# Kernel tuning notes

Measured on AMD Instinct MI355X. Metric: run time of the kernel, lower is better.

Reference implementation:

```python
import jax, jax.numpy as jnp
import numpy as np

B, S, D = 4, 2048, 2048
E = 8            # num_experts
TOP_K = 2
H = 1408         # intermediate_size per expert
SH = 2 * H       # shared expert intermediate (shared_experts=2)


def setup_inputs() -> dict:
    key = jax.random.key(0)
    ks = jax.random.split(key, 8)
    sc = 0.02
    return {
        "hidden_states": jax.random.normal(ks[0], (B, S, D), jnp.float32),
        "gate_w": jax.random.normal(ks[1], (E, D), jnp.float32) * sc,   # torch Linear weight [out,in]
        "w1": jax.random.normal(ks[2], (E, H, D), jnp.float32) * sc,    # gate_proj per expert
        "w3": jax.random.normal(ks[3], (E, H, D), jnp.float32) * sc,    # up_proj per expert
        "w2": jax.random.normal(ks[4], (E, D, H), jnp.float32) * sc,    # down_proj per expert
        "sw1": jax.random.normal(ks[5], (SH, D), jnp.float32) * sc,
        "sw3": jax.random.normal(ks[6], (SH, D), jnp.float32) * sc,
        "sw2": jax.random.normal(ks[7], (D, SH), jnp.float32) * sc,
    }


def reference(hidden_states, gate_w, w1, w3, w2, sw1, sw3, sw2):
    b, s, d = hidden_states.shape
    x = hidden_states.reshape(-1, d)                      # [T, D]
    logits = x @ gate_w.T                                 # [T, E]
    rw, sel = jax.lax.top_k(logits, TOP_K)                # [T, K]
    rw = jax.nn.softmax(rw, axis=-1)                      # norm_topk_prob=True
    onehot = jax.nn.one_hot(sel, E, dtype=x.dtype)        # [T, K, E]
    token_mask = onehot.sum(axis=1)                       # [T, E] in {0,1}
    # NOTE: faithful to the source quirk: expert_weights.sum(dim=-1) on a flat
    # masked gather sums routing weights over ALL tokens selecting the expert,
    # producing one scalar per expert.
    s_e = (rw[..., None] * onehot).sum(axis=(0, 1))       # [E]
    combine = token_mask * s_e                            # [T, E]
    # per-expert SwiGLU MLP on all tokens (dense combine form of gather/scatter)
    g = jnp.einsum('td,ehd->eth', x, w1)                  # [E, T, H]
    u = jnp.einsum('td,ehd->eth', x, w3)
    a = jax.nn.silu(g) * u
    y = jnp.einsum('eth,edh->etd', a, w2)                 # [E, T, D]
    out = jnp.einsum('te,etd->td', combine, y)            # [T, D]
    shared = (jax.nn.silu(x @ sw1.T) * (x @ sw3.T)) @ sw2.T
    out = out + shared
    return out.reshape(b, s, d)
```

## Files before the change

### kernel.cpp

```cpp
#include <hip/hip_runtime.h>
#include <hip/hip_bf16.h>
#include <stdint.h>

#define T_TOK 8192
#define DIM   2048
#define NEXP  8
#define HDIM  1408
#define SHDIM 2816

typedef __attribute__((ext_vector_type(8))) short bfrag;
typedef __attribute__((ext_vector_type(4))) float f32x4;
typedef __attribute__((ext_vector_type(4))) short s16x4;

__device__ __forceinline__ short f2bf(float f) {
    union { float f; uint32_t u; } v; v.f = f;
    return (short)((v.u + 0x8000u) >> 16);
}
__device__ __forceinline__ float bf2f(short s) {
    union { uint32_t u; float f; } v; v.u = ((uint32_t)(uint16_t)s) << 16;
    return v.f;
}

__device__ __forceinline__ bfrag cvt8(float4 a, float4 b) {
    bfrag r;
    r[0] = f2bf(a.x); r[1] = f2bf(a.y); r[2] = f2bf(a.z); r[3] = f2bf(a.w);
    r[4] = f2bf(b.x); r[5] = f2bf(b.y); r[6] = f2bf(b.z); r[7] = f2bf(b.w);
    return r;
}

__device__ __forceinline__ void gload16(const void* g, void* l) {
    __builtin_amdgcn_global_load_lds(
        (__attribute__((address_space(1))) void*)(g),
        (__attribute__((address_space(3))) void*)(l), 16, 0, 0);
}

#define MFMA16(a, b, c) __builtin_amdgcn_mfma_f32_16x16x32_bf16((a), (b), (c), 0, 0, 0)


__global__ __launch_bounds__(256) void gate_cvt_kernel(
    const float* __restrict__ x, const float* __restrict__ gw,
    __hip_bfloat16* __restrict__ xbf,
    int* __restrict__ sel, int* __restrict__ meta, float* __restrict__ s_e,
    const float* __restrict__ sw1f, const float* __restrict__ sw3f,
    const float* __restrict__ sw2f,
    __hip_bfloat16* __restrict__ sw1bf, __hip_bfloat16* __restrict__ sw3bf,
    __hip_bfloat16* __restrict__ sw2bf)
{
    const int bid = blockIdx.x;
    if (bid >= T_TOK / 32) {
        constexpr size_t E_SW = (size_t)SHDIM * DIM;
        constexpr int NCH = (int)(3 * E_SW / 2048);
        const int w = bid - T_TOK / 32;
        for (int c = w; c < NCH; c += 256) {
            size_t elem = (size_t)c * 2048 + threadIdx.x * 8;
            const float* s; __hip_bfloat16* d;
            if      (elem < E_SW)     { s = sw1f + elem;             d = sw1bf + elem; }
            else if (elem < 2 * E_SW) { s = sw3f + (elem - E_SW);    d = sw3bf + (elem - E_SW); }
            else                      { s = sw2f + (elem - 2 * E_SW); d = sw2bf + (elem - 2 * E_SW); }
            float4 a = ((const float4*)s)[0], b = ((const float4*)s)[1];
            *(bfrag*)d = cvt8(a, b);
        }
        return;
    }
    __shared__ float g[NEXP * DIM];
    for (int i = threadIdx.x; i < NEXP * DIM; i += 256) g[i] = gw[i];
    __syncthreads();
    const int wid = threadIdx.x >> 6, lane = threadIdx.x & 63;
    for (int it = 0; it < 8; ++it) {
        const int t = bid * 32 + wid * 8 + it;
        float acc[NEXP];
#pragma unroll
        for (int e = 0; e < NEXP; ++e) acc[e] = 0.f;
        const float4* xr = (const float4*)(x + (size_t)t * DIM);
        for (int j = 0; j < DIM / 4; j += 64) {
            float4 xv = xr[j + lane];
            s16x4 xv16 = { f2bf(xv.x), f2bf(xv.y), f2bf(xv.z), f2bf(xv.w) };
            *(s16x4*)&xbf[(size_t)t * DIM + (j + lane) * 4] = xv16;
#pragma unroll
            for (int e = 0; e < NEXP; ++e) {
                float4 gv = *(const float4*)&g[e * DIM + (j + lane) * 4];
                acc[e] += xv.x * gv.x + xv.y * gv.y + xv.z * gv.z + xv.w * gv.w;
            }
        }
#pragma unroll
        for (int e = 0; e < NEXP; ++e)
            for (int o = 32; o; o >>= 1) acc[e] += __shfl_xor(acc[e], o);
        if (lane == 0) {
            int e0 = 0; float v0 = acc[0];
#pragma unroll
            for (int e = 1; e < NEXP; ++e) if (acc[e] > v0) { v0 = acc[e]; e0 = e; }
            int e1 = -1; float v1 = -3.4e38f;
#pragma unroll
            for (int e = 0; e < NEXP; ++e) if (e != e0 && acc[e] > v1) { v1 = acc[e]; e1 = e; }
            float p0 = 1.f / (1.f + __expf(v1 - v0));
            float p1 = 1.f - p0;
            sel[2 * t] = e0; sel[2 * t + 1] = e1;
            atomicAdd(&s_e[e0], p0); atomicAdd(&s_e[e1], p1);
            atomicAdd(&meta[e0], 1); atomicAdd(&meta[e1], 1);
        }
    }
}

__global__ void scan_kernel(int* meta) {
    if (threadIdx.x == 0) {
        int acc = 0;
        for (int e = 0; e < NEXP; ++e) {
            meta[16 + e] = acc;
            meta[8 + e]  = acc;
            acc += meta[e];
        }
        meta[24] = acc;
    }
}

__global__ __launch_bounds__(256) void fill_kernel(
    const int* __restrict__ sel, int* __restrict__ meta,
    int* __restrict__ list, int2* __restrict__ slots)
{
    const int t = blockIdx.x * 256 + threadIdx.x;
    int e0 = sel[2 * t], e1 = sel[2 * t + 1];
    int p0 = atomicAdd(&meta[8 + e0], 1); list[p0] = t;
    int p1 = atomicAdd(&meta[8 + e1], 1); list[p1] = t;
    slots[t] = make_int2(p0, p1);
}


template<int N, bool GATHER>
__device__ __forceinline__ void up_core(
    const __hip_bfloat16* __restrict__ X,
    const __hip_bfloat16* __restrict__ B1p,
    const __hip_bfloat16* __restrict__ B3p,
    __hip_bfloat16* __restrict__ actp,
    const int* __restrict__ list,
    int base, int count, int m0, int n0, short* lds)
{
    constexpr int K = DIM;
    constexpr int NT = K / 64;
    short (*As)[256 * 64]  = (short (*)[256 * 64])lds;
    short (*B1s)[128 * 64] = (short (*)[128 * 64])(lds + 32768);
    short (*B3s)[128 * 64] = (short (*)[128 * 64])(lds + 49152);

    const int tid = threadIdx.x, wid = tid >> 6, lane = tid & 63;
    const int rlo = lane >> 3;
    const int swslot = (lane & 7) ^ rlo;

    const __hip_bfloat16* pA[4];
#pragma unroll
    for (int q = 0; q < 4; ++q) {
        int row = (q * 8 + wid) * 8 + rlo;
        int r = m0 + row; if (r > count - 1) r = count - 1;
        int ga = GATHER ? list[base + r] : r;
        pA[q] = X + (size_t)ga * K + swslot * 8;
    }
    const __hip_bfloat16* pB1[2];
    const __hip_bfloat16* pB3[2];
#pragma unroll
    for (int q = 0; q < 2; ++q) {
        int row = (q * 8 + wid) * 8 + rlo;
        pB1[q] = B1p + (size_t)(n0 + row) * K + swslot * 8;
        pB3[q] = B3p + (size_t)(n0 + row) * K + swslot * 8;
    }

#define STAGE_UP(T, BUF) do { const int k0_ = (T) * 64;                         \
    _Pragma("unroll") for (int q = 0; q < 4; ++q)                               \
        gload16(pA[q] + k0_, &As[BUF][(q * 8 + wid) * 512]);                    \
    _Pragma("unroll") for (int q = 0; q < 2; ++q) {                             \
        gload16(pB1[q] + k0_, &B1s[BUF][(q * 8 + wid) * 512]);                  \
        gload16(pB3[q] + k0_, &B3s[BUF][(q * 8 + wid) * 512]); } } while (0)

    const int wm = wid >> 2, wn = wid & 3;
    const int l15 = lane & 15, lhi = lane >> 4;

    f32x4 accg[8][2], accu[8][2];
#pragma unroll
    for (int i = 0; i < 8; ++i)
#pragma unroll
        for (int j = 0; j < 2; ++j) { accg[i][j] = 0.f; accu[i][j] = 0.f; }

    STAGE_UP(0, 0);
    __syncthreads();
    int cur = 0;
#pragma unroll 1
    for (int t = 0; t < NT; ++t) {
        if (t + 1 < NT) STAGE_UP(t + 1, cur ^ 1);
        __builtin_amdgcn_sched_barrier(0);
        bfrag b1f[2][2], b3f[2][2];
#pragma unroll
        for (int j = 0; j < 2; ++j)
#pragma unroll
            for (int kk = 0; kk < 2; ++kk) {
                int rb = wn * 32 + j * 16 + l15;
                int c = kk * 4 + lhi;
                int off = rb * 128 + ((c ^ (rb & 7)) << 4);
                b1f[j][kk] = *(const bfrag*)((const char*)B1s[cur] + off);
                b3f[j][kk] = *(const bfrag*)((const char*)B3s[cur] + off);
            }
        __builtin_amdgcn_s_setprio(1);
#pragma unroll
        for (int i = 0; i < 8; ++i) {
            int ra = wm * 128 + i * 16 + l15;
            const char* abase = (const char*)As[cur] + ra * 128;
            bfrag a0 = *(const bfrag*)(abase + ((lhi       ^ (ra & 7)) << 4));
            bfrag a1 = *(const bfrag*)(abase + (((4 + lhi) ^ (ra & 7)) << 4));
#pragma unroll
            for (int j = 0; j < 2; ++j) {
                accg[i][j] = MFMA16(a0, b1f[j][0], accg[i][j]);
                accu[i][j] = MFMA16(a0, b3f[j][0], accu[i][j]);
                accg[i][j] = MFMA16(a1, b1f[j][1], accg[i][j]);
                accu[i][j] = MFMA16(a1, b3f[j][1], accu[i][j]);
            }
        }
        __builtin_amdgcn_s_setprio(0);
        __syncthreads();
        cur ^= 1;
    }
#undef STAGE_UP

#pragma unroll
    for (int i = 0; i < 8; ++i)
#pragma unroll
        for (int r = 0; r < 4; ++r) {
            int m = wm * 128 + i * 16 + lhi * 4 + r;
            if (m0 + m < count) {
#pragma unroll
                for (int j = 0; j < 2; ++j) {
                    float gg = accg[i][j][r];
                    float uu = accu[i][j][r];
                    float a = gg / (1.f + __expf(-gg)) * uu;
                    int n = n0 + wn * 32 + j * 16 + l15;
                    actp[(size_t)(base + m0 + m) * N + n] = __float2bfloat16(a);
                }
            }
        }
}

template<int KD, bool TO_BF16>
__device__ __forceinline__ void down_core(
    const __hip_bfloat16* __restrict__ Ap,
    const __hip_bfloat16* __restrict__ Bp,
    float* __restrict__ out, __hip_bfloat16* __restrict__ yscr,
    int base, int count, int m0, int n0, short* lds)
{
    constexpr int NT = KD / 64;
    short (*As)[256 * 64] = (short (*)[256 * 64])lds;
    short (*Bs)[256 * 64] = (short (*)[256 * 64])(lds + 32768);

    const int tid = threadIdx.x, wid = tid >> 6, lane = tid & 63;
    const int rlo = lane >> 3;
    const int swslot = (lane & 7) ^ rlo;

    const __hip_bfloat16* pA[4];
    const __hip_bfloat16* pB[4];
#pragma unroll
    for (int q = 0; q < 4; ++q) {
        int row = (q * 8 + wid) * 8 + rlo;
        int r = m0 + row; if (r > count - 1) r = count - 1;
        pA[q] = Ap + (size_t)(base + r) * KD + swslot * 8;
        pB[q] = Bp + (size_t)(n0 + row) * KD + swslot * 8;
    }

#define STAGE_DN(T, BUF) do { const int k0_ = (T) * 64;                         \
    _Pragma("unroll") for (int q = 0; q < 4; ++q) {                             \
        gload16(pA[q] + k0_, &As[BUF][(q * 8 + wid) * 512]);                    \
        gload16(pB[q] + k0_, &Bs[BUF][(q * 8 + wid) * 512]); } } while (0)

    const int wm = wid >> 2, wn = wid & 3;
    const int l15 = lane & 15, lhi = lane >> 4;

    f32x4 acc[8][4];
#pragma unroll
    for (int i = 0; i < 8; ++i)
#pragma unroll
        for (int j = 0; j < 4; ++j) acc[i][j] = 0.f;

    STAGE_DN(0, 0);
    __syncthreads();
    int cur = 0;
#pragma unroll 1
    for (int t = 0; t < NT; ++t) {
        if (t + 1 < NT) STAGE_DN(t + 1, cur ^ 1);
        __builtin_amdgcn_sched_barrier(0);
        bfrag bf[4][2];
#pragma unroll
        for (int j = 0; j < 4; ++j)
#pragma unroll
            for (int kk = 0; kk < 2; ++kk) {
                int rb = wn * 64 + j * 16 + l15;
                int c = kk * 4 + lhi;
                bf[j][kk] = *(const bfrag*)((const char*)Bs[cur] + rb * 128 + ((c ^ (rb & 7)) << 4));
            }
        __builtin_amdgcn_s_setprio(1);
#pragma unroll
        for (int i = 0; i < 8; ++i) {
            int ra = wm * 128 + i * 16 + l15;
            const char* abase = (const char*)As[cur] + ra * 128;
            bfrag a0 = *(const bfrag*)(abase + ((lhi       ^ (ra & 7)) << 4));
            bfrag a1 = *(const bfrag*)(abase + (((4 + lhi) ^ (ra & 7)) << 4));
#pragma unroll
            for (int j = 0; j < 4; ++j) {
                acc[i][j] = MFMA16(a0, bf[j][0], acc[i][j]);
                acc[i][j] = MFMA16(a1, bf[j][1], acc[i][j]);
            }
        }
        __builtin_amdgcn_s_setprio(0);
        __syncthreads();
        cur ^= 1;
    }
#undef STAGE_DN

#pragma unroll
    for (int i = 0; i < 8; ++i)
#pragma unroll
        for (int r = 0; r < 4; ++r) {
            int m = wm * 128 + i * 16 + lhi * 4 + r;
            if (m0 + m < count) {
#pragma unroll
                for (int j = 0; j < 4; ++j) {
                    int n = n0 + wn * 64 + j * 16 + l15;
                    if (TO_BF16)
                        yscr[(size_t)(base + m0 + m) * DIM + n] = __float2bfloat16(acc[i][j][r]);
                    else
                        out[(size_t)(m0 + m) * DIM + n] = acc[i][j][r];
                }
            }
        }
}

#define UPSH_NG 704
#define UPSH_NCVT 384
__global__ __launch_bounds__(512, 2) void upsh_cvt_k(
    const __hip_bfloat16* __restrict__ X,
    const __hip_bfloat16* __restrict__ SW1, const __hip_bfloat16* __restrict__ SW3,
    __hip_bfloat16* __restrict__ act_sh,
    const float* __restrict__ w1f, const float* __restrict__ w3f,
    __hip_bfloat16* __restrict__ w1bf, __hip_bfloat16* __restrict__ w3bf)
{
    const int bid = blockIdx.x;
    if (bid >= UPSH_NG) {
        constexpr size_t E_W = (size_t)NEXP * HDIM * DIM;
        constexpr int NCH = (int)(2 * E_W / 4096);
        const int w = bid - UPSH_NG;
        for (int c = w; c < NCH; c += UPSH_NCVT) {
            size_t elem = (size_t)c * 4096 + threadIdx.x * 8;
            const float* s; __hip_bfloat16* d;
            if (elem < E_W) { s = w1f + elem;         d = w1bf + elem; }
            else            { s = w3f + (elem - E_W); d = w3bf + (elem - E_W); }
            float4 a = ((const float4*)s)[0], b = ((const float4*)s)[1];
            *(bfrag*)d = cvt8(a, b);
        }
        return;
    }
    constexpr int nx = SHDIM / 128, cpx = UPSH_NG / 8;
    const int virt = (bid & 7) * cpx + (bid >> 3);
    const int xi = virt % nx, yi = virt / nx;
    __shared__ alignas(16) short lds[65536];
    up_core<SHDIM, false>(X, SW1, SW3, act_sh, nullptr, 0, T_TOK, yi * 256, xi * 128, lds);
}

template<int KD, bool TO_BF16>
__global__ __launch_bounds__(512, 2) void down_k(
    const __hip_bfloat16* __restrict__ A, const __hip_bfloat16* __restrict__ W2,
    float* __restrict__ out, __hip_bfloat16* __restrict__ yscr,
    const int* __restrict__ meta)
{
    constexpr int nx = DIM / 256, ny = T_TOK / 256, nz = TO_BF16 ? NEXP : 1;
    constexpr int nwg = nx * ny * nz, cpx = nwg / 8;
    const int bid = (int)blockIdx.x + nx * ((int)blockIdx.y + ny * (int)blockIdx.z);
    const int virt = (bid & 7) * cpx + (bid >> 3);
    const int xi = virt % nx, rest = virt / nx, yi = rest % ny, e = rest / ny;
    int count, base;
    if (TO_BF16) { count = meta[e]; base = meta[16 + e]; if (yi * 256 >= count) return; }
    else { count = T_TOK; base = 0; }
    __shared__ alignas(16) short lds[65536];
    down_core<KD, TO_BF16>(A, W2 + (size_t)e * DIM * KD, out, yscr,
                           base, count, yi * 256, xi * 256, lds);
}

template<int N, bool GATHER>
__global__ __launch_bounds__(512, 2) void up_k(
    const __hip_bfloat16* __restrict__ X,
    const __hip_bfloat16* __restrict__ W1, const __hip_bfloat16* __restrict__ W3,
    __hip_bfloat16* __restrict__ act,
    const int* __restrict__ list, const int* __restrict__ meta)
{
    constexpr int nx = N / 128, ny = T_TOK / 256, nz = GATHER ? NEXP : 1;
    constexpr int nwg = nx * ny * nz, cpx = nwg / 8;
    const int bid = (int)blockIdx.x + nx * ((int)blockIdx.y + ny * (int)blockIdx.z);
    const int virt = (bid & 7) * cpx + (bid >> 3);
    const int xi = virt % nx, rest = virt / nx, yi = rest % ny, e = rest / ny;
    int count, base;
    if (GATHER) { count = meta[e]; base = meta[16 + e]; if (yi * 256 >= count) return; }
    else { count = T_TOK; base = 0; }
    __shared__ alignas(16) short lds[65536];
    up_core<N, GATHER>(X, W1 + (size_t)e * N * DIM, W3 + (size_t)e * N * DIM,
                       act, list, base, count, yi * 256, xi * 128, lds);
}

__global__ __launch_bounds__(256) void cvt_w2_kernel(
    const float* __restrict__ w2f, __hip_bfloat16* __restrict__ w2bf)
{
    constexpr size_t E_W = (size_t)NEXP * HDIM * DIM;
    const int stride = gridDim.x * 256;
    for (size_t i = blockIdx.x * 256 + threadIdx.x; i < E_W / 8; i += stride) {
        const float4* p = (const float4*)(w2f + i * 8);
        float4 a = p[0], b = p[1];
        *(bfrag*)(w2bf + i * 8) = cvt8(a, b);
    }
}

#define MID_NDS 256
#define MID_NUE 2816
#define MID_NCVT 256
__global__ __launch_bounds__(512, 2) void mid_merged(
    const __hip_bfloat16* __restrict__ act_sh, const __hip_bfloat16* __restrict__ sw2bf,
    float* __restrict__ out,
    const __hip_bfloat16* __restrict__ xbf,
    const __hip_bfloat16* __restrict__ w1bf, const __hip_bfloat16* __restrict__ w3bf,
    __hip_bfloat16* __restrict__ act_ex,
    const int* __restrict__ list, const int* __restrict__ meta,
    const float* __restrict__ w2f, __hip_bfloat16* __restrict__ w2bf)
{
    const int bid = (int)blockIdx.x;
    if (bid >= MID_NDS + MID_NUE) {
        constexpr size_t E_W = (size_t)NEXP * HDIM * DIM;
        constexpr int NCH = (int)(E_W / 4096);
        const int w = bid - (MID_NDS + MID_NUE);
        for (int c = w; c < NCH; c += MID_NCVT) {
            size_t elem = (size_t)c * 4096 + threadIdx.x * 8;
            float4 a = ((const float4*)(w2f + elem))[0];
            float4 b = ((const float4*)(w2f + elem))[1];
            *(bfrag*)(w2bf + elem) = cvt8(a, b);
        }
        return;
    }
    __shared__ alignas(16) short lds[65536];
    if (bid < MID_NDS) {
        constexpr int cpx = MID_NDS / 8;
        const int virt = (bid & 7) * cpx + (bid >> 3);
        const int n0 = (virt & 7) * 256, m0 = (virt >> 3) * 256;
        down_core<SHDIM, false>(act_sh, sw2bf, out, nullptr, 0, T_TOK, m0, n0, lds);
    } else {
        const int b = bid - MID_NDS;
        constexpr int cpx = MID_NUE / 8;
        const int virt = (b & 7) * cpx + (b >> 3);
        const int e = virt / 352, r = virt % 352;
        const int n0 = (r % 11) * 128, m0 = (r / 11) * 256;
        const int count = meta[e], base = meta[16 + e];
        if (m0 >= count) return;
        up_core<HDIM, true>(xbf, w1bf + (size_t)e * HDIM * DIM, w3bf + (size_t)e * HDIM * DIM,
                            act_ex, list, base, count, m0, n0, lds);
    }
}

__global__ __launch_bounds__(256) void combine_kernel(
    float* __restrict__ out, const __hip_bfloat16* __restrict__ yscr,
    const int* __restrict__ sel, const int2* __restrict__ slots,
    const float* __restrict__ s_e)
{
    const int t = blockIdx.x;
    const int d = threadIdx.x * 8;
    const int2 sl = slots[t];
    const float se0 = s_e[sel[2 * t]];
    const float se1 = s_e[sel[2 * t + 1]];
    bfrag y0 = *(const bfrag*)&yscr[(size_t)sl.x * DIM + d];
    bfrag y1 = *(const bfrag*)&yscr[(size_t)sl.y * DIM + d];
    float4* o = (float4*)(out + (size_t)t * DIM + d);
    float4 o0 = o[0], o1 = o[1];
    o0.x += se0 * bf2f(y0[0]) + se1 * bf2f(y1[0]);
    o0.y += se0 * bf2f(y0[1]) + se1 * bf2f(y1[1]);
    o0.z += se0 * bf2f(y0[2]) + se1 * bf2f(y1[2]);
    o0.w += se0 * bf2f(y0[3]) + se1 * bf2f(y1[3]);
    o1.x += se0 * bf2f(y0[4]) + se1 * bf2f(y1[4]);
    o1.y += se0 * bf2f(y0[5]) + se1 * bf2f(y1[5]);
    o1.z += se0 * bf2f(y0[6]) + se1 * bf2f(y1[6]);
    o1.w += se0 * bf2f(y0[7]) + se1 * bf2f(y1[7]);
    o[0] = o0; o[1] = o1;
}

extern "C" void kernel_launch(void* const* d_in, const int* in_sizes, int n_in,
                              void* d_out, int out_size, void* d_ws, size_t ws_size,
                              hipStream_t stream) {
    const float* x   = (const float*)d_in[0];
    const float* gw  = (const float*)d_in[1];
    const float* w1  = (const float*)d_in[2];
    const float* w3  = (const float*)d_in[3];
    const float* w2  = (const float*)d_in[4];
    const float* sw1 = (const float*)d_in[5];
    const float* sw3 = (const float*)d_in[6];
    const float* sw2 = (const float*)d_in[7];
    float* out = (float*)d_out;

    const size_t SZ_X    = (size_t)T_TOK * DIM * 2;
    const size_t SZ_W    = (size_t)NEXP * HDIM * DIM * 2;
    const size_t SZ_SW   = (size_t)SHDIM * DIM * 2;
    const size_t SZ_ACTS = (size_t)T_TOK * SHDIM * 2;
    const size_t SZ_ACTE = (size_t)2 * T_TOK * HDIM * 2;
    const size_t SZ_INTS = (size_t)6 * T_TOK * sizeof(int) + 512;
    const size_t need_base   = SZ_X + 3 * SZ_W + 3 * SZ_SW + SZ_ACTS + SZ_INTS;
    const size_t need_merged = need_base + SZ_ACTE;

    char* p = (char*)d_ws;
    __hip_bfloat16* xbf   = (__hip_bfloat16*)p; p += SZ_X;
    __hip_bfloat16* w1bf  = (__hip_bfloat16*)p; p += SZ_W;
    __hip_bfloat16* w3bf  = (__hip_bfloat16*)p; p += SZ_W;
    __hip_bfloat16* w2bf  = (__hip_bfloat16*)p; p += SZ_W;
    __hip_bfloat16* sw1bf = (__hip_bfloat16*)p; p += SZ_SW;
    __hip_bfloat16* sw3bf = (__hip_bfloat16*)p; p += SZ_SW;
    __hip_bfloat16* sw2bf = (__hip_bfloat16*)p; p += SZ_SW;
    __hip_bfloat16* act_sh = (__hip_bfloat16*)p; p += SZ_ACTS;
    const bool merged = (need_merged <= ws_size);
    __hip_bfloat16* act_ex = merged ? (__hip_bfloat16*)p : act_sh;
    if (merged) p += SZ_ACTE;
    int*  list  = (int*)p;  p += (size_t)2 * T_TOK * sizeof(int);
    int*  sel   = (int*)p;  p += (size_t)2 * T_TOK * sizeof(int);
    int2* slots = (int2*)p; p += (size_t)2 * T_TOK * sizeof(int);
    int*  meta  = (int*)p;
    float* s_e  = (float*)(meta + 32);
    __hip_bfloat16* yscr = (__hip_bfloat16*)d_ws;
    if (need_base > ws_size) return;

    hipMemsetAsync(meta, 0, 256, stream);
    gate_cvt_kernel<<<T_TOK / 32 + 256, 256, 0, stream>>>(
        x, gw, xbf, sel, meta, s_e, sw1, sw3, sw2, sw1bf, sw3bf, sw2bf);
    scan_kernel<<<1, 64, 0, stream>>>(meta);
    fill_kernel<<<T_TOK / 256, 256, 0, stream>>>(sel, meta, list, slots);

    upsh_cvt_k<<<UPSH_NG + UPSH_NCVT, 512, 0, stream>>>(
        xbf, sw1bf, sw3bf, act_sh, w1, w3, w1bf, w3bf);

    if (merged) {
        mid_merged<<<MID_NDS + MID_NUE + MID_NCVT, 512, 0, stream>>>(
            act_sh, sw2bf, out, xbf, w1bf, w3bf, act_ex, list, meta, w2, w2bf);
        down_k<HDIM, true><<<dim3(DIM / 256, T_TOK / 256, NEXP), 512, 0, stream>>>(
            act_ex, w2bf, out, yscr, meta);
    } else {
        cvt_w2_kernel<<<2048, 256, 0, stream>>>(w2, w2bf);
        down_k<SHDIM, false><<<dim3(DIM / 256, T_TOK / 256, 1), 512, 0, stream>>>(
            act_sh, sw2bf, out, nullptr, meta);
        up_k<HDIM, true><<<dim3(HDIM / 128, T_TOK / 256, NEXP), 512, 0, stream>>>(
            xbf, w1bf, w3bf, act_ex, list, meta);
        down_k<HDIM, true><<<dim3(DIM / 256, T_TOK / 256, NEXP), 512, 0, stream>>>(
            act_ex, w2bf, out, yscr, meta);
    }
    combine_kernel<<<T_TOK, 256, 0, stream>>>(out, yscr, sel, slots, s_e);
}
```

Before: 963.9 us.

## Fuse expert combine into down-projection epilogue via scaled atomic scatter

The routed-expert down-projection epilogue now scales each result by the expert's routing scalar and atomically adds it straight into the output row of the owning token. This removes the bf16 y scratch buffer, the slots array and the separate combine kernel, saving a launch plus the write and re-read of a token-by-dim intermediate. In exchange it issues many scattered fp32 atomics to global memory, which can contend. Summation order also becomes nondeterministic, although the precision loss from rounding y to bf16 is gone.

After: 1.022 ms. +6.0%, slower.

```diff
diff --git a/kernel.cpp b/kernel.cpp
--- a/kernel.cpp
+++ b/kernel.cpp
@@ -15,10 +15,6 @@
 __device__ __forceinline__ short f2bf(float f) {
     union { float f; uint32_t u; } v; v.f = f;
     return (short)((v.u + 0x8000u) >> 16);
-}
-__device__ __forceinline__ float bf2f(short s) {
-    union { uint32_t u; float f; } v; v.u = ((uint32_t)(uint16_t)s) << 16;
-    return v.f;
 }
 
 __device__ __forceinline__ bfrag cvt8(float4 a, float4 b) {
@@ -54,8 +50,8 @@
         for (int c = w; c < NCH; c += 256) {
             size_t elem = (size_t)c * 2048 + threadIdx.x * 8;
             const float* s; __hip_bfloat16* d;
-            if      (elem < E_SW)     { s = sw1f + elem;             d = sw1bf + elem; }
-            else if (elem < 2 * E_SW) { s = sw3f + (elem - E_SW);    d = sw3bf + (elem - E_SW); }
+            if      (elem < E_SW)     { s = sw1f + elem;              d = sw1bf + elem; }
+            else if (elem < 2 * E_SW) { s = sw3f + (elem - E_SW);     d = sw3bf + (elem - E_SW); }
             else                      { s = sw2f + (elem - 2 * E_SW); d = sw2bf + (elem - 2 * E_SW); }
             float4 a = ((const float4*)s)[0], b = ((const float4*)s)[1];
             *(bfrag*)d = cvt8(a, b);
@@ -114,14 +110,12 @@
 }
 
 __global__ __launch_bounds__(256) void fill_kernel(
-    const int* __restrict__ sel, int* __restrict__ meta,
-    int* __restrict__ list, int2* __restrict__ slots)
+    const int* __restrict__ sel, int* __restrict__ meta, int* __restrict__ list)
 {
     const int t = blockIdx.x * 256 + threadIdx.x;
     int e0 = sel[2 * t], e1 = sel[2 * t + 1];
     int p0 = atomicAdd(&meta[8 + e0], 1); list[p0] = t;
     int p1 = atomicAdd(&meta[8 + e1], 1); list[p1] = t;
-    slots[t] = make_int2(p0, p1);
 }
 
 
@@ -234,11 +228,12 @@
         }
 }
 
-template<int KD, bool TO_BF16>
+template<int KD, bool SCATTER>
 __device__ __forceinline__ void down_core(
     const __hip_bfloat16* __restrict__ Ap,
     const __hip_bfloat16* __restrict__ Bp,
-    float* __restrict__ out, __hip_bfloat16* __restrict__ yscr,
+    float* __restrict__ out,
+    const int* __restrict__ list, float scale,
     int base, int count, int m0, int n0, short* lds)
 {
     constexpr int NT = KD / 64;
@@ -314,13 +309,14 @@
         for (int r = 0; r < 4; ++r) {
             int m = wm * 128 + i * 16 + lhi * 4 + r;
             if (m0 + m < count) {
+                const int trow = SCATTER ? list[base + m0 + m] : (m0 + m);
 #pragma unroll
                 for (int j = 0; j < 4; ++j) {
                     int n = n0 + wn * 64 + j * 16 + l15;
-                    if (TO_BF16)
-                        yscr[(size_t)(base + m0 + m) * DIM + n] = __float2bfloat16(acc[i][j][r]);
+                    if (SCATTER)
+                        atomicAdd(&out[(size_t)trow * DIM + n], acc[i][j][r] * scale);
                     else
-                        out[(size_t)(m0 + m) * DIM + n] = acc[i][j][r];
+                        out[(size_t)trow * DIM + n] = acc[i][j][r];
                 }
             }
         }
@@ -357,22 +353,23 @@
     up_core<SHDIM, false>(X, SW1, SW3, act_sh, nullptr, 0, T_TOK, yi * 256, xi * 128, lds);
 }
 
-template<int KD, bool TO_BF16>
+template<int KD, bool SCATTER>
 __global__ __launch_bounds__(512, 2) void down_k(
     const __hip_bfloat16* __restrict__ A, const __hip_bfloat16* __restrict__ W2,
-    float* __restrict__ out, __hip_bfloat16* __restrict__ yscr,
-    const int* __restrict__ meta)
-{
-    constexpr int nx = DIM / 256, ny = T_TOK / 256, nz = TO_BF16 ? NEXP : 1;
+    float* __restrict__ out, const int* __restrict__ list,
+    const int* __restrict__ meta, const float* __restrict__ s_e)
+{
+    constexpr int nx = DIM / 256, ny = T_TOK / 256, nz = SCATTER ? NEXP : 1;
     constexpr int nwg = nx * ny * nz, cpx = nwg / 8;
     const int bid = (int)blockIdx.x + nx * ((int)blockIdx.y + ny * (int)blockIdx.z);
     const int virt = (bid & 7) * cpx + (bid >> 3);
     const int xi = virt % nx, rest = virt / nx, yi = rest % ny, e = rest / ny;
     int count, base;
-    if (TO_BF16) { count = meta[e]; base = meta[16 + e]; if (yi * 256 >= count) return; }
+    if (SCATTER) { count = meta[e]; base = meta[16 + e]; if (yi * 256 >= count) return; }
     else { count = T_TOK; base = 0; }
+    const float scale = SCATTER ? s_e[e] : 1.0f;
     __shared__ alignas(16) short lds[65536];
-    down_core<KD, TO_BF16>(A, W2 + (size_t)e * DIM * KD, out, yscr,
+    down_core<KD, SCATTER>(A, W2 + (size_t)e * DIM * KD, out, list, scale,
                            base, count, yi * 256, xi * 256, lds);
 }
 
@@ -438,7 +435,7 @@
         constexpr int cpx = MID_NDS / 8;
         const int virt = (bid & 7) * cpx + (bid >> 3);
         const int n0 = (virt & 7) * 256, m0 = (virt >> 3) * 256;
-        down_core<SHDIM, false>(act_sh, sw2bf, out, nullptr, 0, T_TOK, m0, n0, lds);
+        down_core<SHDIM, false>(act_sh, sw2bf, out, nullptr, 1.0f, 0, T_TOK, m0, n0, lds);
     } else {
         const int b = bid - MID_NDS;
         constexpr int cpx = MID_NUE / 8;
@@ -450,31 +447,6 @@
         up_core<HDIM, true>(xbf, w1bf + (size_t)e * HDIM * DIM, w3bf + (size_t)e * HDIM * DIM,
                             act_ex, list, base, count, m0, n0, lds);
     }
-}
-
-__global__ __launch_bounds__(256) void combine_kernel(
-    float* __restrict__ out, const __hip_bfloat16* __restrict__ yscr,
-    const int* __restrict__ sel, const int2* __restrict__ slots,
-    const float* __restrict__ s_e)
-{
-    const int t = blockIdx.x;
-    const int d = threadIdx.x * 8;
-    const int2 sl = slots[t];
-    const float se0 = s_e[sel[2 * t]];
-    const float se1 = s_e[sel[2 * t + 1]];
-    bfrag y0 = *(const bfrag*)&yscr[(size_t)sl.x * DIM + d];
-    bfrag y1 = *(const bfrag*)&yscr[(size_t)sl.y * DIM + d];
-    float4* o = (float4*)(out + (size_t)t * DIM + d);
-    float4 o0 = o[0], o1 = o[1];
-    o0.x += se0 * bf2f(y0[0]) + se1 * bf2f(y1[0]);
-    o0.y += se0 * bf2f(y0[1]) + se1 * bf2f(y1[1]);
-    o0.z += se0 * bf2f(y0[2]) + se1 * bf2f(y1[2]);
-    o0.w += se0 * bf2f(y0[3]) + se1 * bf2f(y1[3]);
-    o1.x += se0 * bf2f(y0[4]) + se1 * bf2f(y1[4]);
-    o1.y += se0 * bf2f(y0[5]) + se1 * bf2f(y1[5]);
-    o1.z += se0 * bf2f(y0[6]) + se1 * bf2f(y1[6]);
-    o1.w += se0 * bf2f(y0[7]) + se1 * bf2f(y1[7]);
-    o[0] = o0; o[1] = o1;
 }
 
 extern "C" void kernel_launch(void* const* d_in, const int* in_sizes, int n_in,
@@ -495,7 +467,7 @@
     const size_t SZ_SW   = (size_t)SHDIM * DIM * 2;
     const size_t SZ_ACTS = (size_t)T_TOK * SHDIM * 2;
     const size_t SZ_ACTE = (size_t)2 * T_TOK * HDIM * 2;
-    const size_t SZ_INTS = (size_t)6 * T_TOK * sizeof(int) + 512;
+    const size_t SZ_INTS = (size_t)4 * T_TOK * sizeof(int) + 512;
     const size_t need_base   = SZ_X + 3 * SZ_W + 3 * SZ_SW + SZ_ACTS + SZ_INTS;
     const size_t need_merged = need_base + SZ_ACTE;
 
@@ -513,17 +485,15 @@
     if (merged) p += SZ_ACTE;
     int*  list  = (int*)p;  p += (size_t)2 * T_TOK * sizeof(int);
     int*  sel   = (int*)p;  p += (size_t)2 * T_TOK * sizeof(int);
-    int2* slots = (int2*)p; p += (size_t)2 * T_TOK * sizeof(int);
     int*  meta  = (int*)p;
     float* s_e  = (float*)(meta + 32);
-    __hip_bfloat16* yscr = (__hip_bfloat16*)d_ws;
     if (need_base > ws_size) return;
 
     hipMemsetAsync(meta, 0, 256, stream);
     gate_cvt_kernel<<<T_TOK / 32 + 256, 256, 0, stream>>>(
         x, gw, xbf, sel, meta, s_e, sw1, sw3, sw2, sw1bf, sw3bf, sw2bf);
     scan_kernel<<<1, 64, 0, stream>>>(meta);
-    fill_kernel<<<T_TOK / 256, 256, 0, stream>>>(sel, meta, list, slots);
+    fill_kernel<<<T_TOK / 256, 256, 0, stream>>>(sel, meta, list);
 
     upsh_cvt_k<<<UPSH_NG + UPSH_NCVT, 512, 0, stream>>>(
         xbf, sw1bf, sw3bf, act_sh, w1, w3, w1bf, w3bf);
@@ -532,15 +502,14 @@
         mid_merged<<<MID_NDS + MID_NUE + MID_NCVT, 512, 0, stream>>>(
             act_sh, sw2bf, out, xbf, w1bf, w3bf, act_ex, list, meta, w2, w2bf);
         down_k<HDIM, true><<<dim3(DIM / 256, T_TOK / 256, NEXP), 512, 0, stream>>>(
-            act_ex, w2bf, out, yscr, meta);
+            act_ex, w2bf, out, list, meta, s_e);
     } else {
         cvt_w2_kernel<<<2048, 256, 0, stream>>>(w2, w2bf);
         down_k<SHDIM, false><<<dim3(DIM / 256, T_TOK / 256, 1), 512, 0, stream>>>(
-            act_sh, sw2bf, out, nullptr, meta);
+            act_sh, sw2bf, out, nullptr, meta, s_e);
         up_k<HDIM, true><<<dim3(HDIM / 128, T_TOK / 256, NEXP), 512, 0, stream>>>(
             xbf, w1bf, w3bf, act_ex, list, meta);
         down_k<HDIM, true><<<dim3(DIM / 256, T_TOK / 256, NEXP), 512, 0, stream>>>(
-            act_ex, w2bf, out, yscr, meta);
-    }
-    combine_kernel<<<T_TOK, 256, 0, stream>>>(out, yscr, sel, slots, s_e);
-}
+            act_ex, w2bf, out, list, meta, s_e);
+    }
+}
```
